# Optimization experiments

Measured on AMD Instinct MI355X. Metric: run time of the kernel, lower is better.

Reference implementation:

```python
import jax, jax.numpy as jnp
import numpy as np

DIM = 1024
HEADS = 16
DIM_HEAD = 64
INNER = HEADS * DIM_HEAD  # 1024
FEAT = 1024  # cfg.different_learnable_tokens=False -> feature_dim = dim
EPS = 1e-5
SCALE = 1.0 / np.sqrt(DIM_HEAD)


def setup_inputs() -> dict:
    key = jax.random.key(0)
    ks = jax.random.split(key, 10)
    b, n = 2, 2048
    x = jax.random.normal(ks[0], (b, n, DIM), jnp.float32)
    y = jax.random.normal(ks[1], (b, n, FEAT), jnp.float32)
    # learned parameters
    ln_g = jnp.ones((DIM,), jnp.float32)
    ln_b = jnp.zeros((DIM,), jnp.float32)
    w_qkv = jax.random.normal(ks[2], (DIM, 3 * INNER), jnp.float32) * (DIM ** -0.5)
    w_av = jax.random.normal(ks[3], (FEAT, INNER), jnp.float32) * (FEAT ** -0.5)
    w_out = jax.random.normal(ks[4], (INNER, DIM), jnp.float32) * (INNER ** -0.5)
    b_out = jnp.zeros((DIM,), jnp.float32)
    w_yout = jax.random.normal(ks[5], (INNER, FEAT), jnp.float32) * (INNER ** -0.5)
    b_yout = jnp.zeros((FEAT,), jnp.float32)
    return {"x": x, "y": y, "ln_g": ln_g, "ln_b": ln_b, "w_qkv": w_qkv,
            "w_av": w_av, "w_out": w_out, "b_out": b_out,
            "w_yout": w_yout, "b_yout": b_yout}


def _split_heads(t):  # [b,n,(h d)] -> [b,h,n,d]
    b, n, _ = t.shape
    return t.reshape(b, n, HEADS, DIM_HEAD).transpose(0, 2, 1, 3)


def _merge_heads(t):  # [b,h,n,d] -> [b,n,(h d)]
    b, h, n, d = t.shape
    return t.transpose(0, 2, 1, 3).reshape(b, n, h * d)


def reference(x, y, ln_g, ln_b, w_qkv, w_av, w_out, b_out, w_yout, b_yout):
    # LayerNorm
    mu = jnp.mean(x, axis=-1, keepdims=True)
    var = jnp.mean(jnp.square(x - mu), axis=-1, keepdims=True)
    xn = (x - mu) * jax.lax.rsqrt(var + EPS) * ln_g + ln_b

    qkv = xn @ w_qkv  # [b,n,3*inner]
    q, k, v = jnp.split(qkv, 3, axis=-1)
    av = y @ w_av  # [b,n,inner]
    q, k, v, av = map(_split_heads, (q, k, v, av))  # [b,h,n,d]

    # shared QK softmax, applied to both V and another_v
    scores = jnp.einsum('bhnd,bhmd->bhnm', q, k) * SCALE
    attn = jax.nn.softmax(scores, axis=-1)
    x_ctx = jnp.einsum('bhnm,bhmd->bhnd', attn, v)
    y_ctx = jnp.einsum('bhnm,bhmd->bhnd', attn, av)

    x_out = _merge_heads(x_ctx) @ w_out + b_out
    y_out = _merge_heads(y_ctx) @ w_yout + b_yout
    return (x_out, y_out)
```

## Files before the change

### kernel.cpp

```cpp
#include <hip/hip_runtime.h>

typedef _Float16 half8 __attribute__((ext_vector_type(8)));
typedef _Float16 half4v __attribute__((ext_vector_type(4)));
typedef __fp16 fp16x2 __attribute__((ext_vector_type(2)));
typedef float f32x4 __attribute__((ext_vector_type(4)));
typedef unsigned int u32;

#define SEQ 2048
#define NTOK 4096
#define DM 1024
#define QKS 2048
#define LN_EPS 1e-5f
#define LOG2E_SCALE 0.18033688f

typedef const __attribute__((address_space(1))) u32* gas_ptr;
typedef __attribute__((address_space(3))) u32* las_ptr;
__device__ __forceinline__ void gld_lds16(const void* g, void* l) {
  __builtin_amdgcn_global_load_lds((gas_ptr)g, (las_ptr)l, 16, 0, 0);
}

#define BARRIER() do { __builtin_amdgcn_s_barrier(); __builtin_amdgcn_sched_barrier(0); } while (0)
#define VMW(N) asm volatile("s_waitcnt vmcnt(" #N ")" ::: "memory")
#define LGW() do { asm volatile("s_waitcnt lgkmcnt(0)" ::: "memory"); __builtin_amdgcn_sched_barrier(0); } while (0)

__global__ __launch_bounds__(256) void prep_kernel(
    const float* __restrict__ x, const float* __restrict__ g, const float* __restrict__ bta,
    const float* __restrict__ y,
    const float* __restrict__ w_qkv, const float* __restrict__ w_av,
    const float* __restrict__ w_out, const float* __restrict__ w_yout,
    _Float16* __restrict__ xn, _Float16* __restrict__ yh,
    _Float16* __restrict__ wqkvT, _Float16* __restrict__ wavT,
    _Float16* __restrict__ woutT, _Float16* __restrict__ wyoutT) {
  __shared__ float smem[64 * 65];
  const int bid = blockIdx.x;
  const int t = threadIdx.x;
  if (bid < 4096) {
    const int row = bid;
    const float4 v = ((const float4*)(x + (size_t)row * DM))[t];
    float s = v.x + v.y + v.z + v.w;
#pragma unroll
    for (int m = 1; m < 64; m <<= 1) s += __shfl_xor(s, m, 64);
    float* red = smem;
    const int wid = t >> 6, lane = t & 63;
    if (lane == 0) red[wid] = s;
    __syncthreads();
    const float mu = (red[0] + red[1] + red[2] + red[3]) * (1.0f / DM);
    const float dx = v.x - mu, dy = v.y - mu, dz = v.z - mu, dw = v.w - mu;
    float ss = dx * dx + dy * dy + dz * dz + dw * dw;
#pragma unroll
    for (int m = 1; m < 64; m <<= 1) ss += __shfl_xor(ss, m, 64);
    __syncthreads();
    if (lane == 0) red[wid] = ss;
    __syncthreads();
    const float var = (red[0] + red[1] + red[2] + red[3]) * (1.0f / DM);
    const float rstd = rsqrtf(var + LN_EPS);
    const float4 gg = ((const float4*)g)[t];
    const float4 bb = ((const float4*)bta)[t];
    half4v o;
    o[0] = (_Float16)(dx * rstd * gg.x + bb.x);
    o[1] = (_Float16)(dy * rstd * gg.y + bb.y);
    o[2] = (_Float16)(dz * rstd * gg.z + bb.z);
    o[3] = (_Float16)(dw * rstd * gg.w + bb.w);
    *(half4v*)(xn + (size_t)row * DM + t * 4) = o;
  } else if (bid < 8192) {
    const int row = bid - 4096;
    const float4 v = ((const float4*)(y + (size_t)row * DM))[t];
    half4v o;
    o[0] = (_Float16)v.x; o[1] = (_Float16)v.y;
    o[2] = (_Float16)v.z; o[3] = (_Float16)v.w;
    *(half4v*)(yh + (size_t)row * DM + t * 4) = o;
  } else {
    const int id2 = bid - 8192;
    const float* W; _Float16* WT; int Nc, bx, by;
    if (id2 < 768) { W = w_qkv; WT = wqkvT; Nc = 3072; bx = id2 % 48; by = id2 / 48; }
    else {
      const int id3 = id2 - 768, sel = id3 >> 8;
      Nc = 1024; bx = id3 & 15; by = (id3 >> 4) & 15;
      if (sel == 0) { W = w_av; WT = wavT; }
      else if (sel == 1) { W = w_out; WT = woutT; }
      else { W = w_yout; WT = wyoutT; }
    }
    float (*tile)[65] = (float(*)[65])smem;
    const int n0 = bx * 64, k0 = by * 64;
    const int c = t & 63;
#pragma unroll
    for (int i = 0; i < 16; i++) {
      const int r = (t >> 6) * 16 + i;
      tile[r][c] = W[(size_t)(k0 + r) * Nc + n0 + c];
    }
    __syncthreads();
#pragma unroll
    for (int i = 0; i < 16; i++) {
      const int n = (t >> 6) * 16 + i;
      WT[(size_t)(n0 + n) * 1024 + k0 + c] = (_Float16)tile[c][n];
    }
  }
}

__global__ __launch_bounds__(512, 2) void gemm8p_kernel(
    const _Float16* __restrict__ xn, const _Float16* __restrict__ wqkvT,
    const _Float16* __restrict__ yh, const _Float16* __restrict__ wavT,
    _Float16* __restrict__ qkvm, _Float16* __restrict__ vtb,
    _Float16* __restrict__ avtb) {
  __shared__ _Float16 Ab[2][8192];
  __shared__ _Float16 Bb[2][8192];
  const int swz = ((blockIdx.x & 7) << 5) + (blockIdx.x >> 3);
  const _Float16 *A, *B;
  int m0, n0, isav;
  if (swz < 192) { A = xn; B = wqkvT; m0 = (swz / 12) * 256; n0 = (swz % 12) * 256; isav = 0; }
  else { const int u = swz - 192; A = yh; B = wavT; m0 = (u >> 2) * 256; n0 = (u & 3) * 256; isav = 1; }
  const int t = threadIdx.x;
  const int wid = t >> 6, lane = t & 63, lo = lane & 15, hi = lane >> 4;
  const int wm = wid >> 2, wn = wid & 3;
  const int srow = t >> 2;
  const int sx = ((t & 3) ^ (srow & 3)) << 3;
  const _Float16* gA = A + (size_t)(m0 + srow) * 1024 + sx;
  const _Float16* gB = B + (size_t)(n0 + srow) * 1024 + sx;
  const int rdz = (hi ^ (lo & 3)) << 3;
  const int arow = (wm * 128 + lo) * 32 + rdz;
  const int brow = (wn * 64 + lo) * 32 + rdz;

  f32x4 acc[8][4];
#pragma unroll
  for (int i = 0; i < 8; i++)
#pragma unroll
    for (int j = 0; j < 4; j++) {
      acc[i][j][0] = 0.f; acc[i][j][1] = 0.f; acc[i][j][2] = 0.f; acc[i][j][3] = 0.f;
    }
  half8 af[4], bf[4];

#define STG_A(BUF, HH, KT) gld_lds16(gA + (HH) * 131072 + (KT) * 32, &Ab[BUF][(HH) * 4096 + t * 8])
#define STG_B(BUF, HH, KT) gld_lds16(gB + (HH) * 131072 + (KT) * 32, &Bb[BUF][(HH) * 4096 + t * 8])
#define RDA(BUF, FB)                                                     \
  _Pragma("unroll") for (int f2 = 0; f2 < 4; f2++)                       \
      af[f2] = *(const half8*)&Ab[BUF][arow + ((FB) + f2) * 512]
#define RDB(BUF, G0)                                                     \
  _Pragma("unroll") for (int g2 = 0; g2 < 2; g2++)                       \
      bf[(G0) + g2] = *(const half8*)&Bb[BUF][brow + ((G0) + g2) * 512]
#define MMA(FB, G0)                                                      \
  do {                                                                   \
    __builtin_amdgcn_s_setprio(1);                                       \
    _Pragma("unroll") for (int f2 = 0; f2 < 4; f2++)                     \
        _Pragma("unroll") for (int g2 = 0; g2 < 2; g2++)                 \
            acc[(FB) + f2][(G0) + g2] = __builtin_amdgcn_mfma_f32_16x16x32_f16( \
                af[f2], bf[(G0) + g2], acc[(FB) + f2][(G0) + g2], 0, 0, 0); \
    __builtin_amdgcn_s_setprio(0);                                       \
  } while (0)

  STG_A(0, 0, 0); STG_A(0, 1, 0); STG_B(0, 0, 0); STG_B(0, 1, 0);
  STG_A(1, 0, 1);

  for (int it = 0; it < 16; it++) {
    const int T1 = 2 * it + 1;
    const int N0 = (2 * it + 2) & 31, N1 = (2 * it + 3) & 31;
    VMW(1); BARRIER();
    RDA(0, 0); RDB(0, 0);
    STG_A(1, 1, T1);
    LGW(); MMA(0, 0);
    BARRIER(); RDB(0, 2); STG_B(1, 0, T1); LGW(); MMA(0, 2);
    BARRIER(); RDA(0, 4); STG_B(1, 1, T1); LGW(); MMA(4, 2);
    BARRIER(); STG_A(0, 0, N0); MMA(4, 0);
    VMW(1); BARRIER();
    RDA(1, 0); RDB(1, 0);
    STG_A(0, 1, N0);
    LGW(); MMA(0, 0);
    BARRIER(); RDB(1, 2); STG_B(0, 0, N0); LGW(); MMA(0, 2);
    BARRIER(); RDA(1, 4); STG_B(0, 1, N0); LGW(); MMA(4, 2);
    BARRIER(); STG_A(1, 0, N1); MMA(4, 0);
  }
#undef STG_A
#undef STG_B
#undef RDA
#undef RDB
#undef MMA

#pragma unroll
  for (int f = 0; f < 8; f++)
#pragma unroll
    for (int g = 0; g < 4; g++)
#pragma unroll
      for (int r = 0; r < 4; r++) {
        const int row = m0 + wm * 128 + f * 16 + 4 * hi + r;
        const int col = n0 + wn * 64 + g * 16 + lo;
        const _Float16 v = (_Float16)acc[f][g][r];
        if (!isav && col < 2048) {
          qkvm[(size_t)row * QKS + col] = v;
        } else {
          const int coff = isav ? col : col - 2048;
          _Float16* Ct = isav ? avtb : vtb;
          Ct[(((size_t)((row >> 11) << 4) + (coff >> 6)) * 64 + (coff & 63)) * SEQ +
             (row & (SEQ - 1))] = v;
        }
      }
}

__global__ __launch_bounds__(256) void gemmout_kernel(
    const _Float16* __restrict__ A0, const _Float16* __restrict__ B0,
    float* F0, const float* bias0, int nblk0,
    const _Float16* __restrict__ A1, const _Float16* __restrict__ B1,
    float* F1, const float* bias1) {
  __shared__ _Float16 As[128 * 32];
  __shared__ _Float16 Bs[128 * 32];
  int id = ((blockIdx.x & 7) * (gridDim.x >> 3)) + (blockIdx.x >> 3);
  const _Float16 *A, *BT;
  float* Cf; const float* bias;
  if (id < nblk0) { A = A0; BT = B0; Cf = F0; bias = bias0; }
  else { id -= nblk0; A = A1; BT = B1; Cf = F1; bias = bias1; }
  const int bx = id & 7, by = id >> 3;
  const int t = threadIdx.x;
  const int wid = t >> 6, lane = t & 63, lo = lane & 15, hi = lane >> 4;
  const int wm = wid >> 1, wn = wid & 1;
  const int m0 = by * 128, n0 = bx * 128;
  const int K = 1024;

  f32x4 acc[4][4];
#pragma unroll
  for (int i = 0; i < 4; i++)
#pragma unroll
    for (int j = 0; j < 4; j++) {
      acc[i][j][0] = 0.f; acc[i][j][1] = 0.f; acc[i][j][2] = 0.f; acc[i][j][3] = 0.f;
    }
  const int rowA = t >> 2;
  const int kcol = (t & 3) * 8;
  const _Float16* gA = A + (size_t)(m0 + rowA) * K + kcol;
  const _Float16* gB = BT + (size_t)(n0 + rowA) * K + kcol;

  for (int k0 = 0; k0 < K; k0 += 32) {
#pragma unroll
    for (int j = 0; j < 2; j++) {
      gld_lds16(gA + (size_t)(j * 64) * K + k0, As + j * 2048 + wid * 512);
      gld_lds16(gB + (size_t)(j * 64) * K + k0, Bs + j * 2048 + wid * 512);
    }
    __syncthreads();
    half8 af[4], bf[4];
#pragma unroll
    for (int i = 0; i < 4; i++) {
      af[i] = *(const half8*)(As + (wm * 64 + i * 16 + lo) * 32 + hi * 8);
      bf[i] = *(const half8*)(Bs + (wn * 64 + i * 16 + lo) * 32 + hi * 8);
    }
#pragma unroll
    for (int i = 0; i < 4; i++)
#pragma unroll
      for (int j = 0; j < 4; j++)
        acc[i][j] = __builtin_amdgcn_mfma_f32_16x16x32_f16(af[i], bf[j], acc[i][j], 0, 0, 0);
    __syncthreads();
  }
#pragma unroll
  for (int i = 0; i < 4; i++)
#pragma unroll
    for (int j = 0; j < 4; j++)
#pragma unroll
      for (int r = 0; r < 4; r++) {
        const int row = m0 + wm * 64 + i * 16 + 4 * hi + r;
        const int col = n0 + wn * 64 + j * 16 + lo;
        Cf[(size_t)row * 1024 + col] = acc[i][j][r] + bias[col];
      }
}

__global__ __launch_bounds__(256) void attn_kernel(
    const _Float16* __restrict__ qkvm,
    const _Float16* __restrict__ vt,
    const _Float16* __restrict__ avt,
    _Float16* __restrict__ xctx, _Float16* __restrict__ yctx) {
  __shared__ _Float16 Kl[2][4096];
  __shared__ _Float16 Vl[2][4096];
  __shared__ _Float16 Al[2][4096];
  __shared__ _Float16 Pl[4][2048];

  const int t = threadIdx.x;
  const int wid = t >> 6, lane = t & 63, lo = lane & 15, hi = lane >> 4;
  const int l7 = lane & 7;
  const int id = blockIdx.x;
  const int bh = ((id & 7) << 2) + ((id >> 3) >> 4);
  const int qt = (id >> 3) & 15;
  const int b = bh >> 4, h = bh & 15;
  const int q0 = qt * 128 + wid * 32;
  const size_t tokbase = (size_t)b * SEQ;
  const _Float16* vbase = vt + (size_t)bh * 64 * SEQ;
  const _Float16* abase = avt + (size_t)bh * 64 * SEQ;

  half8 qf[2][2];
#pragma unroll
  for (int rg = 0; rg < 2; rg++)
#pragma unroll
    for (int kc = 0; kc < 2; kc++)
      qf[rg][kc] = *(const half8*)(qkvm + (tokbase + q0 + rg * 16 + lo) * QKS +
                                   h * 64 + kc * 32 + hi * 8);

  f32x4 zero;
  zero[0] = 0.f; zero[1] = 0.f; zero[2] = 0.f; zero[3] = 0.f;
  f32x4 accx[2][4], accy[2][4];
  float mC[2], lsum[2];
#pragma unroll
  for (int rg = 0; rg < 2; rg++) {
#pragma unroll
    for (int j = 0; j < 4; j++) { accx[rg][j] = zero; accy[rg][j] = zero; }
    mC[rg] = -1.0e30f; lsum[rg] = 0.0f;
  }

  const int skey = t >> 3;
  const int sc7 = t & 7;

#define STAGE(kv0, BSEL)                                                          \
  do {                                                                            \
    _Pragma("unroll") for (int j = 0; j < 2; j++) {                               \
      const int key = skey + j * 32;                                              \
      const int cs = ((sc7 ^ (key & 7)) << 3);                                    \
      gld_lds16(qkvm + (tokbase + (kv0) + key) * QKS + DM + h * 64 + cs,          \
                &Kl[BSEL][j * 2048 + wid * 512]);                                 \
      gld_lds16(vbase + (size_t)key * SEQ + (kv0) + cs,                           \
                &Vl[BSEL][j * 2048 + wid * 512]);                                 \
      gld_lds16(abase + (size_t)key * SEQ + (kv0) + cs,                           \
                &Al[BSEL][j * 2048 + wid * 512]);                                 \
    }                                                                             \
  } while (0)

#define BODY(BSEL)                                                                \
  do {                                                                            \
    const _Float16* Kb = Kl[BSEL];                                                \
    const _Float16* Vb = Vl[BSEL];                                                \
    const _Float16* Ab2 = Al[BSEL];                                               \
    _Float16* Pw = Pl[wid];                                                       \
    f32x4 s[2][4];                                                                \
    _Pragma("unroll") for (int kg = 0; kg < 4; kg++) {                            \
      const int kr = (kg * 16 + lo) * 64;                                         \
      const half8 ak0 = *(const half8*)(Kb + kr + ((hi ^ l7) << 3));              \
      const half8 ak1 = *(const half8*)(Kb + kr + (((4 | hi) ^ l7) << 3));        \
      _Pragma("unroll") for (int rg = 0; rg < 2; rg++) {                          \
        f32x4 z = __builtin_amdgcn_mfma_f32_16x16x32_f16(ak0, qf[rg][0], zero, 0, 0, 0); \
        s[rg][kg] = __builtin_amdgcn_mfma_f32_16x16x32_f16(ak1, qf[rg][1], z, 0, 0, 0);  \
      }                                                                           \
    }                                                                             \
    float tmC[2];                                                                 \
    _Pragma("unroll") for (int rg = 0; rg < 2; rg++) {                            \
      float a0 = fmaxf(fmaxf(s[rg][0][0], s[rg][0][1]), fmaxf(s[rg][0][2], s[rg][0][3])); \
      float a1 = fmaxf(fmaxf(s[rg][1][0], s[rg][1][1]), fmaxf(s[rg][1][2], s[rg][1][3])); \
      float a2 = fmaxf(fmaxf(s[rg][2][0], s[rg][2][1]), fmaxf(s[rg][2][2], s[rg][2][3])); \
      float a3 = fmaxf(fmaxf(s[rg][3][0], s[rg][3][1]), fmaxf(s[rg][3][2], s[rg][3][3])); \
      float tm = fmaxf(fmaxf(a0, a1), fmaxf(a2, a3));                             \
      tm = fmaxf(tm, __shfl_xor(tm, 16, 64));                                     \
      tm = fmaxf(tm, __shfl_xor(tm, 32, 64));                                     \
      tmC[rg] = tm * LOG2E_SCALE;                                                 \
    }                                                                             \
    const bool grow = (tmC[0] > mC[0] + 8.0f) | (tmC[1] > mC[1] + 8.0f);          \
    if (__any(grow)) {                                                            \
      float fcs[2];                                                               \
      _Pragma("unroll") for (int rg = 0; rg < 2; rg++) {                          \
        const float mn = fmaxf(mC[rg], tmC[rg]);                                  \
        fcs[rg] = exp2f(mC[rg] - mn);                                             \
        mC[rg] = mn;                                                              \
        lsum[rg] *= fcs[rg];                                                      \
      }                                                                           \
      _Pragma("unroll") for (int rg = 0; rg < 2; rg++)                            \
        _Pragma("unroll") for (int r = 0; r < 4; r++) {                           \
          const float fcb = __shfl(fcs[rg], 4 * hi + r, 64);                      \
          _Pragma("unroll") for (int ng = 0; ng < 4; ng++) {                      \
            accx[rg][ng][r] *= fcb;                                               \
            accy[rg][ng][r] *= fcb;                                               \
          }                                                                       \
        }                                                                         \
    }                                                                             \
    _Pragma("unroll") for (int rg = 0; rg < 2; rg++) {                            \
      float rs = 0.0f;                                                            \
      _Pragma("unroll") for (int kg = 0; kg < 4; kg++) {                          \
        const float p0 = exp2f(fmaf(s[rg][kg][0], LOG2E_SCALE, -mC[rg]));         \
        const float p1 = exp2f(fmaf(s[rg][kg][1], LOG2E_SCALE, -mC[rg]));         \
        const float p2 = exp2f(fmaf(s[rg][kg][2], LOG2E_SCALE, -mC[rg]));         \
        const float p3 = exp2f(fmaf(s[rg][kg][3], LOG2E_SCALE, -mC[rg]));         \
        rs += (p0 + p1) + (p2 + p3);                                              \
        const fp16x2 c01 = __builtin_amdgcn_cvt_pkrtz(p0, p1);                    \
        const fp16x2 c23 = __builtin_amdgcn_cvt_pkrtz(p2, p3);                    \
        half4v pk;                                                                \
        pk[0] = (_Float16)c01[0]; pk[1] = (_Float16)c01[1];                       \
        pk[2] = (_Float16)c23[0]; pk[3] = (_Float16)c23[1];                       \
        *(half4v*)(Pw + (rg * 16 + lo) * 64 +                                     \
                   (((kg * 2 + (hi >> 1)) ^ l7) << 3) + ((hi & 1) << 2)) = pk;    \
      }                                                                           \
      lsum[rg] += rs;                                                             \
    }                                                                             \
    __builtin_amdgcn_s_setprio(1);                                                \
    _Pragma("unroll") for (int kk = 0; kk < 2; kk++) {                            \
      half8 pa[2];                                                                \
      _Pragma("unroll") for (int rg = 0; rg < 2; rg++)                            \
        pa[rg] = *(const half8*)(Pw + (rg * 16 + lo) * 64 + (((kk * 4 + hi) ^ l7) << 3)); \
      _Pragma("unroll") for (int ng = 0; ng < 4; ng++) {                          \
        const int vr = (ng * 16 + lo) * 64 + (((kk * 4 + hi) ^ l7) << 3);         \
        const half8 bv = *(const half8*)(Vb + vr);                                \
        const half8 ba = *(const half8*)(Ab2 + vr);                               \
        _Pragma("unroll") for (int rg = 0; rg < 2; rg++) {                        \
          accx[rg][ng] = __builtin_amdgcn_mfma_f32_16x16x32_f16(pa[rg], bv, accx[rg][ng], 0, 0, 0); \
          accy[rg][ng] = __builtin_amdgcn_mfma_f32_16x16x32_f16(pa[rg], ba, accy[rg][ng], 0, 0, 0); \
        }                                                                         \
      }                                                                           \
    }                                                                             \
    __builtin_amdgcn_s_setprio(0);                                                \
  } while (0)

  STAGE(0, 0);
  for (int tt = 0; tt < SEQ / 64; tt += 2) {
    __syncthreads();
    STAGE((tt + 1) * 64, 1);
    BODY(0);
    __syncthreads();
    if (tt + 2 < SEQ / 64) STAGE((tt + 2) * 64, 0);
    BODY(1);
  }
#undef STAGE
#undef BODY

#pragma unroll
  for (int rg = 0; rg < 2; rg++) {
    lsum[rg] += __shfl_xor(lsum[rg], 16, 64);
    lsum[rg] += __shfl_xor(lsum[rg], 32, 64);
  }
#pragma unroll
  for (int rg = 0; rg < 2; rg++) {
    const float inv = 1.0f / lsum[rg];
#pragma unroll
    for (int r = 0; r < 4; r++) {
      const float invb = __shfl(inv, 4 * hi + r, 64);
      const size_t tok = tokbase + q0 + rg * 16 + 4 * hi + r;
#pragma unroll
      for (int ng = 0; ng < 4; ng++) {
        const int col = h * 64 + ng * 16 + lo;
        xctx[tok * DM + col] = (_Float16)(accx[rg][ng][r] * invb);
        yctx[tok * DM + col] = (_Float16)(accy[rg][ng][r] * invb);
      }
    }
  }
}

extern "C" void kernel_launch(void* const* d_in, const int* in_sizes, int n_in,
                              void* d_out, int out_size, void* d_ws, size_t ws_size,
                              hipStream_t stream) {
  const float* x      = (const float*)d_in[0];
  const float* y      = (const float*)d_in[1];
  const float* ln_g   = (const float*)d_in[2];
  const float* ln_b   = (const float*)d_in[3];
  const float* w_qkv  = (const float*)d_in[4];
  const float* w_av   = (const float*)d_in[5];
  const float* w_out  = (const float*)d_in[6];
  const float* b_out  = (const float*)d_in[7];
  const float* w_yout = (const float*)d_in[8];
  const float* b_yout = (const float*)d_in[9];
  float* out = (float*)d_out;

  _Float16* ws     = (_Float16*)d_ws;
  _Float16* xn     = ws;
  _Float16* yh     = xn + 4194304;
  _Float16* wqkvT  = yh + 4194304;
  _Float16* wavT   = wqkvT + 3145728;
  _Float16* woutT  = wavT + 1048576;
  _Float16* wyoutT = woutT + 1048576;
  _Float16* qkvm   = wyoutT + 1048576;
  _Float16* vtb    = qkvm + 8388608;
  _Float16* avtb   = vtb + 4194304;
  _Float16* xc     = avtb + 4194304;
  _Float16* yc     = xc + 4194304;

  prep_kernel<<<9728, 256, 0, stream>>>(x, ln_g, ln_b, y, w_qkv, w_av, w_out, w_yout,
                                        xn, yh, wqkvT, wavT, woutT, wyoutT);

  gemm8p_kernel<<<256, 512, 0, stream>>>(xn, wqkvT, yh, wavT, qkvm, vtb, avtb);

  attn_kernel<<<512, 256, 0, stream>>>(qkvm, vtb, avtb, xc, yc);

  gemmout_kernel<<<512, 256, 0, stream>>>(
      xc, woutT, out, b_out, 256,
      yc, wyoutT, out + 4194304, b_yout);
}
```

Measured before the change: 240.6 us.

## Load K/V/AV tiles directly from global into registers, drop shared-memory staging

The attention kernel no longer stages K, V and the second value tensor through double-buffered LDS with async global-to-LDS loads and block barriers. Each wave now reads its K, V and AV fragments straight from global memory into registers, prefetching the next K tile while the current softmax runs. This removes the block-wide barriers and LDS traffic for K/V. In exchange, the four waves of a block each load the same K/V data separately, with no cross-wave reuse, and V/AV loads are issued at the top of each iteration with little latency hiding. The row-sum reduction now uses per-iteration shuffles, and the fp16 conversion changes from pkrtz to a plain cast.

```diff
diff --git a/kernel.cpp b/kernel.cpp
--- a/kernel.cpp
+++ b/kernel.cpp
@@ -2,7 +2,6 @@
 
 typedef _Float16 half8 __attribute__((ext_vector_type(8)));
 typedef _Float16 half4v __attribute__((ext_vector_type(4)));
-typedef __fp16 fp16x2 __attribute__((ext_vector_type(2)));
 typedef float f32x4 __attribute__((ext_vector_type(4)));
 typedef unsigned int u32;
 
@@ -262,9 +261,6 @@
     const _Float16* __restrict__ vt,
     const _Float16* __restrict__ avt,
     _Float16* __restrict__ xctx, _Float16* __restrict__ yctx) {
-  __shared__ _Float16 Kl[2][4096];
-  __shared__ _Float16 Vl[2][4096];
-  __shared__ _Float16 Al[2][4096];
   __shared__ _Float16 Pl[4][2048];
 
   const int t = threadIdx.x;
@@ -276,8 +272,7 @@
   const int b = bh >> 4, h = bh & 15;
   const int q0 = qt * 128 + wid * 32;
   const size_t tokbase = (size_t)b * SEQ;
-  const _Float16* vbase = vt + (size_t)bh * 64 * SEQ;
-  const _Float16* abase = avt + (size_t)bh * 64 * SEQ;
+  _Float16* Pw = Pl[wid];
 
   half8 qf[2][2];
 #pragma unroll
@@ -298,121 +293,127 @@
     mC[rg] = -1.0e30f; lsum[rg] = 0.0f;
   }
 
-  const int skey = t >> 3;
-  const int sc7 = t & 7;
-
-#define STAGE(kv0, BSEL)                                                          \
-  do {                                                                            \
-    _Pragma("unroll") for (int j = 0; j < 2; j++) {                               \
-      const int key = skey + j * 32;                                              \
-      const int cs = ((sc7 ^ (key & 7)) << 3);                                    \
-      gld_lds16(qkvm + (tokbase + (kv0) + key) * QKS + DM + h * 64 + cs,          \
-                &Kl[BSEL][j * 2048 + wid * 512]);                                 \
-      gld_lds16(vbase + (size_t)key * SEQ + (kv0) + cs,                           \
-                &Vl[BSEL][j * 2048 + wid * 512]);                                 \
-      gld_lds16(abase + (size_t)key * SEQ + (kv0) + cs,                           \
-                &Al[BSEL][j * 2048 + wid * 512]);                                 \
-    }                                                                             \
-  } while (0)
-
-#define BODY(BSEL)                                                                \
-  do {                                                                            \
-    const _Float16* Kb = Kl[BSEL];                                                \
-    const _Float16* Vb = Vl[BSEL];                                                \
-    const _Float16* Ab2 = Al[BSEL];                                               \
-    _Float16* Pw = Pl[wid];                                                       \
-    f32x4 s[2][4];                                                                \
-    _Pragma("unroll") for (int kg = 0; kg < 4; kg++) {                            \
-      const int kr = (kg * 16 + lo) * 64;                                         \
-      const half8 ak0 = *(const half8*)(Kb + kr + ((hi ^ l7) << 3));              \
-      const half8 ak1 = *(const half8*)(Kb + kr + (((4 | hi) ^ l7) << 3));        \
-      _Pragma("unroll") for (int rg = 0; rg < 2; rg++) {                          \
-        f32x4 z = __builtin_amdgcn_mfma_f32_16x16x32_f16(ak0, qf[rg][0], zero, 0, 0, 0); \
-        s[rg][kg] = __builtin_amdgcn_mfma_f32_16x16x32_f16(ak1, qf[rg][1], z, 0, 0, 0);  \
-      }                                                                           \
-    }                                                                             \
-    float tmC[2];                                                                 \
-    _Pragma("unroll") for (int rg = 0; rg < 2; rg++) {                            \
-      float a0 = fmaxf(fmaxf(s[rg][0][0], s[rg][0][1]), fmaxf(s[rg][0][2], s[rg][0][3])); \
-      float a1 = fmaxf(fmaxf(s[rg][1][0], s[rg][1][1]), fmaxf(s[rg][1][2], s[rg][1][3])); \
-      float a2 = fmaxf(fmaxf(s[rg][2][0], s[rg][2][1]), fmaxf(s[rg][2][2], s[rg][2][3])); \
-      float a3 = fmaxf(fmaxf(s[rg][3][0], s[rg][3][1]), fmaxf(s[rg][3][2], s[rg][3][3])); \
-      float tm = fmaxf(fmaxf(a0, a1), fmaxf(a2, a3));                             \
-      tm = fmaxf(tm, __shfl_xor(tm, 16, 64));                                     \
-      tm = fmaxf(tm, __shfl_xor(tm, 32, 64));                                     \
-      tmC[rg] = tm * LOG2E_SCALE;                                                 \
-    }                                                                             \
-    const bool grow = (tmC[0] > mC[0] + 8.0f) | (tmC[1] > mC[1] + 8.0f);          \
-    if (__any(grow)) {                                                            \
-      float fcs[2];                                                               \
-      _Pragma("unroll") for (int rg = 0; rg < 2; rg++) {                          \
-        const float mn = fmaxf(mC[rg], tmC[rg]);                                  \
-        fcs[rg] = exp2f(mC[rg] - mn);                                             \
-        mC[rg] = mn;                                                              \
-        lsum[rg] *= fcs[rg];                                                      \
-      }                                                                           \
-      _Pragma("unroll") for (int rg = 0; rg < 2; rg++)                            \
-        _Pragma("unroll") for (int r = 0; r < 4; r++) {                           \
-          const float fcb = __shfl(fcs[rg], 4 * hi + r, 64);                      \
-          _Pragma("unroll") for (int ng = 0; ng < 4; ng++) {                      \
-            accx[rg][ng][r] *= fcb;                                               \
-            accy[rg][ng][r] *= fcb;                                               \
-          }                                                                       \
-        }                                                                         \
-    }                                                                             \
-    _Pragma("unroll") for (int rg = 0; rg < 2; rg++) {                            \
-      float rs = 0.0f;                                                            \
-      _Pragma("unroll") for (int kg = 0; kg < 4; kg++) {                          \
-        const float p0 = exp2f(fmaf(s[rg][kg][0], LOG2E_SCALE, -mC[rg]));         \
-        const float p1 = exp2f(fmaf(s[rg][kg][1], LOG2E_SCALE, -mC[rg]));         \
-        const float p2 = exp2f(fmaf(s[rg][kg][2], LOG2E_SCALE, -mC[rg]));         \
-        const float p3 = exp2f(fmaf(s[rg][kg][3], LOG2E_SCALE, -mC[rg]));         \
-        rs += (p0 + p1) + (p2 + p3);                                              \
-        const fp16x2 c01 = __builtin_amdgcn_cvt_pkrtz(p0, p1);                    \
-        const fp16x2 c23 = __builtin_amdgcn_cvt_pkrtz(p2, p3);                    \
-        half4v pk;                                                                \
-        pk[0] = (_Float16)c01[0]; pk[1] = (_Float16)c01[1];                       \
-        pk[2] = (_Float16)c23[0]; pk[3] = (_Float16)c23[1];                       \
-        *(half4v*)(Pw + (rg * 16 + lo) * 64 +                                     \
-                   (((kg * 2 + (hi >> 1)) ^ l7) << 3) + ((hi & 1) << 2)) = pk;    \
-      }                                                                           \
-      lsum[rg] += rs;                                                             \
-    }                                                                             \
-    __builtin_amdgcn_s_setprio(1);                                                \
-    _Pragma("unroll") for (int kk = 0; kk < 2; kk++) {                            \
-      half8 pa[2];                                                                \
-      _Pragma("unroll") for (int rg = 0; rg < 2; rg++)                            \
-        pa[rg] = *(const half8*)(Pw + (rg * 16 + lo) * 64 + (((kk * 4 + hi) ^ l7) << 3)); \
-      _Pragma("unroll") for (int ng = 0; ng < 4; ng++) {                          \
-        const int vr = (ng * 16 + lo) * 64 + (((kk * 4 + hi) ^ l7) << 3);         \
-        const half8 bv = *(const half8*)(Vb + vr);                                \
-        const half8 ba = *(const half8*)(Ab2 + vr);                               \
-        _Pragma("unroll") for (int rg = 0; rg < 2; rg++) {                        \
-          accx[rg][ng] = __builtin_amdgcn_mfma_f32_16x16x32_f16(pa[rg], bv, accx[rg][ng], 0, 0, 0); \
-          accy[rg][ng] = __builtin_amdgcn_mfma_f32_16x16x32_f16(pa[rg], ba, accy[rg][ng], 0, 0, 0); \
-        }                                                                         \
-      }                                                                           \
-    }                                                                             \
-    __builtin_amdgcn_s_setprio(0);                                                \
-  } while (0)
-
-  STAGE(0, 0);
-  for (int tt = 0; tt < SEQ / 64; tt += 2) {
-    __syncthreads();
-    STAGE((tt + 1) * 64, 1);
-    BODY(0);
-    __syncthreads();
-    if (tt + 2 < SEQ / 64) STAGE((tt + 2) * 64, 0);
-    BODY(1);
-  }
-#undef STAGE
-#undef BODY
-
-#pragma unroll
-  for (int rg = 0; rg < 2; rg++) {
-    lsum[rg] += __shfl_xor(lsum[rg], 16, 64);
-    lsum[rg] += __shfl_xor(lsum[rg], 32, 64);
-  }
+  u32 koff[4], voff[4];
+#pragma unroll
+  for (int kg = 0; kg < 4; kg++)
+    koff[kg] = (u32)((b * SEQ + kg * 16 + lo) * QKS + DM + h * 64 + hi * 8);
+#pragma unroll
+  for (int ng = 0; ng < 4; ng++)
+    voff[ng] = (u32)(bh * (64 * SEQ) + (ng * 16 + lo) * SEQ + hi * 8);
+
+  half8 ak[4][2];
+#pragma unroll
+  for (int kg = 0; kg < 4; kg++) {
+    ak[kg][0] = *(const half8*)(qkvm + koff[kg]);
+    ak[kg][1] = *(const half8*)(qkvm + koff[kg] + 32);
+  }
+
+  for (int tt = 0; tt < SEQ / 64; tt++) {
+    half8 vf[4][2], af[4][2];
+#pragma unroll
+    for (int ng = 0; ng < 4; ng++) {
+#pragma unroll
+      for (int kk = 0; kk < 2; kk++) {
+        vf[ng][kk] = *(const half8*)(vt + voff[ng] + kk * 32);
+        af[ng][kk] = *(const half8*)(avt + voff[ng] + kk * 32);
+      }
+    }
+
+    f32x4 s[2][4];
+#pragma unroll
+    for (int kg = 0; kg < 4; kg++) {
+#pragma unroll
+      for (int rg = 0; rg < 2; rg++) {
+        f32x4 z = __builtin_amdgcn_mfma_f32_16x16x32_f16(ak[kg][0], qf[rg][0], zero, 0, 0, 0);
+        s[rg][kg] = __builtin_amdgcn_mfma_f32_16x16x32_f16(ak[kg][1], qf[rg][1], z, 0, 0, 0);
+      }
+    }
+
+#pragma unroll
+    for (int kg = 0; kg < 4; kg++) koff[kg] += 64 * QKS;
+    if (tt + 1 < SEQ / 64) {
+#pragma unroll
+      for (int kg = 0; kg < 4; kg++) {
+        ak[kg][0] = *(const half8*)(qkvm + koff[kg]);
+        ak[kg][1] = *(const half8*)(qkvm + koff[kg] + 32);
+      }
+    }
+
+    float tmC[2];
+#pragma unroll
+    for (int rg = 0; rg < 2; rg++) {
+      float tm = -3.0e38f;
+#pragma unroll
+      for (int kg = 0; kg < 4; kg++)
+#pragma unroll
+        for (int r = 0; r < 4; r++) tm = fmaxf(tm, s[rg][kg][r]);
+      tm = fmaxf(tm, __shfl_xor(tm, 16, 64));
+      tm = fmaxf(tm, __shfl_xor(tm, 32, 64));
+      tmC[rg] = tm * LOG2E_SCALE;
+    }
+
+    const bool grow = (tmC[0] > mC[0] + 8.0f) | (tmC[1] > mC[1] + 8.0f);
+    if (__any(grow)) {
+      float fcs[2];
+#pragma unroll
+      for (int rg = 0; rg < 2; rg++) {
+        const float mn = fmaxf(mC[rg], tmC[rg]);
+        fcs[rg] = exp2f(mC[rg] - mn);
+        mC[rg] = mn;
+        lsum[rg] *= fcs[rg];
+      }
+#pragma unroll
+      for (int rg = 0; rg < 2; rg++)
+#pragma unroll
+        for (int r = 0; r < 4; r++) {
+          const float fcb = __shfl(fcs[rg], 4 * hi + r, 64);
+#pragma unroll
+          for (int ng = 0; ng < 4; ng++) {
+            accx[rg][ng][r] *= fcb;
+            accy[rg][ng][r] *= fcb;
+          }
+        }
+    }
+
+#pragma unroll
+    for (int rg = 0; rg < 2; rg++) {
+      float rs = 0.0f;
+#pragma unroll
+      for (int kg = 0; kg < 4; kg++) {
+        half4v pk;
+#pragma unroll
+        for (int r = 0; r < 4; r++) {
+          const float p = exp2f(fmaf(s[rg][kg][r], LOG2E_SCALE, -mC[rg]));
+          rs += p;
+          pk[r] = (_Float16)p;
+        }
+        *(half4v*)(Pw + (rg * 16 + lo) * 64 +
+                   (((kg * 2 + (hi >> 1)) ^ l7) << 3) + ((hi & 1) << 2)) = pk;
+      }
+      rs += __shfl_xor(rs, 16, 64);
+      rs += __shfl_xor(rs, 32, 64);
+      lsum[rg] += rs;
+    }
+
+#pragma unroll
+    for (int kk = 0; kk < 2; kk++) {
+      half8 pa[2];
+#pragma unroll
+      for (int rg = 0; rg < 2; rg++)
+        pa[rg] = *(const half8*)(Pw + (rg * 16 + lo) * 64 + (((kk * 4 + hi) ^ l7) << 3));
+#pragma unroll
+      for (int ng = 0; ng < 4; ng++) {
+#pragma unroll
+        for (int rg = 0; rg < 2; rg++) {
+          accx[rg][ng] = __builtin_amdgcn_mfma_f32_16x16x32_f16(pa[rg], vf[ng][kk], accx[rg][ng], 0, 0, 0);
+          accy[rg][ng] = __builtin_amdgcn_mfma_f32_16x16x32_f16(pa[rg], af[ng][kk], accy[rg][ng], 0, 0, 0);
+        }
+      }
+    }
+#pragma unroll
+    for (int ng = 0; ng < 4; ng++) voff[ng] += 64;
+  }
+
 #pragma unroll
   for (int rg = 0; rg < 2; rg++) {
     const float inv = 1.0f / lsum[rg];
```

After: 294.2 us. 22.3% more time.
